# Performance work log

Hardware: AMD Instinct MI355X
Metric: run time of the kernel (lower is better)

## Reference

```python
import jax, jax.numpy as jnp
import numpy as np

H = 2048          # hidden_size
HEAD = 64         # head_size
NH = H // HEAD    # n_heads = 32
B, T = 4, 4096
LORA_MIX = 32     # per-branch rank of time_maa low-rank mixer (5 branches)
LORA_DECAY = 64   # rank of decay low-rank mixer


def setup_inputs() -> dict:
    key = jax.random.key(0)
    ks = jax.random.split(key, 24)
    s = 0.02  # small init scale keeps tanh/silu in sane range
    inp = {
        "hidden": jax.random.normal(ks[0], (B, T, H), jnp.float32),
        "attn_x": jax.random.normal(ks[1], (B, H), jnp.float32),
        "attn_kv": jax.random.normal(ks[2], (B, NH, HEAD, HEAD), jnp.float32),
        "ffn_x": jax.random.normal(ks[3], (B, H), jnp.float32),
        "time_maa_x": jax.random.normal(ks[4], (1, 1, H), jnp.float32) * s,
        "time_maa_w": jax.random.normal(ks[5], (1, 1, H), jnp.float32) * s,
        "time_maa_k": jax.random.normal(ks[6], (1, 1, H), jnp.float32) * s,
        "time_maa_v": jax.random.normal(ks[7], (1, 1, H), jnp.float32) * s,
        "time_maa_r": jax.random.normal(ks[8], (1, 1, H), jnp.float32) * s,
        "time_maa_g": jax.random.normal(ks[9], (1, 1, H), jnp.float32) * s,
        "time_maa_w1": jax.random.normal(ks[10], (H, LORA_MIX * 5), jnp.float32) * s,
        "time_maa_w2": jax.random.normal(ks[11], (5, LORA_MIX, H), jnp.float32) * s,
        "time_decay": jax.random.normal(ks[12], (1, 1, H), jnp.float32) * s,
        "time_decay_w1": jax.random.normal(ks[13], (H, LORA_DECAY), jnp.float32) * s,
        "time_decay_w2": jax.random.normal(ks[14], (LORA_DECAY, H), jnp.float32) * s,
        "time_faaaa": jax.random.normal(ks[15], (NH, HEAD), jnp.float32) * s,
        "receptance_w": jax.random.normal(ks[16], (H, H), jnp.float32) * s,
        "key_w": jax.random.normal(ks[17], (H, H), jnp.float32) * s,
        "value_w": jax.random.normal(ks[18], (H, H), jnp.float32) * s,
        "gate_w": jax.random.normal(ks[19], (H, H), jnp.float32) * s,
        "output_w": jax.random.normal(ks[20], (H, H), jnp.float32) * s,
    }
    return inp


def reference(hidden, attn_x, attn_kv, ffn_x,
              time_maa_x, time_maa_w, time_maa_k, time_maa_v, time_maa_r, time_maa_g,
              time_maa_w1, time_maa_w2,
              time_decay, time_decay_w1, time_decay_w2, time_faaaa,
              receptance_w, key_w, value_w, gate_w, output_w):
    b, t, h = hidden.shape
    # token shift: prepend previous chunk's last token state
    shifted = jnp.concatenate([attn_x[:, None, :], hidden[:, :-1, :]], axis=1)  # [B,T,H]
    x = hidden
    xx = shifted - x
    # low-rank data-dependent mixing coefficients (5 branches)
    xxx = x + xx * time_maa_x                                        # [B,T,H]
    xxx = jnp.tanh(xxx.reshape(-1, h) @ time_maa_w1)                 # [B*T, 5*32]
    xxx = xxx.reshape(-1, 5, LORA_MIX).transpose(1, 0, 2)            # [5, B*T, 32]
    xxx = jnp.einsum('fnr,frh->fnh', xxx, time_maa_w2)               # [5, B*T, H]
    xxx = xxx.reshape(5, b, t, h)
    mw, mk, mv, mr, mg = xxx[0], xxx[1], xxx[2], xxx[3], xxx[4]
    # note: source uses additive mix (x + xx + coeff), faithful to code as written
    td_in = x + xx + (time_maa_w + mw)
    k_in = x + xx + (time_maa_k + mk)
    v_in = x + xx + (time_maa_v + mv)
    r_in = x + xx + (time_maa_r + mr)
    g_in = x + xx + (time_maa_g + mg)
    receptance = jnp.einsum('bth,hd->btd', r_in, receptance_w)
    key = jnp.einsum('bth,hd->btd', k_in, key_w)
    value = jnp.einsum('bth,hd->btd', v_in, value_w)
    gate = jax.nn.silu(jnp.einsum('bth,hd->btd', g_in, gate_w))
    td = jnp.tanh(jnp.einsum('bth,hr->btr', td_in, time_decay_w1))
    td = jnp.einsum('btr,rh->bth', td, time_decay_w2)
    td = time_decay + td                                              # [B,T,H] per-channel decay
    attn_x_new = hidden[:, -1]                                        # [B,H]
    return (receptance, key, value, gate, td, attn_x_new)
```

## Files before the change

kernel.cpp:

```cpp
#include <hip/hip_runtime.h>

#define H 2048
#define TT 4096
#define BB 4
#define NROWS (BB * TT)
#define NTH ((size_t)NROWS * H)
#define KCAT (H + 32)
#define KC8  (H + 64)
#define NTH64 ((size_t)NROWS * 64)

typedef __attribute__((ext_vector_type(8))) short bh8;
typedef __attribute__((ext_vector_type(4))) float f32x4;

__device__ inline unsigned short f2bf(float f) {
    union { float f; unsigned u; } v; v.f = f;
    unsigned r = v.u + 0x7fff + ((v.u >> 16) & 1);
    return (unsigned short)(r >> 16);
}
__device__ inline float bf2f(unsigned short u) {
    union { unsigned u; float f; } v; v.u = ((unsigned)u) << 16; return v.f;
}
__device__ inline void gload_lds16(const void* g, void* l) {
    __builtin_amdgcn_global_load_lds(
        (const __attribute__((address_space(1))) void*)g,
        (__attribute__((address_space(3))) void*)l, 16, 0, 0);
}

__global__ __launch_bounds__(256) void prep_kernel(
    const float* __restrict__ hidden, const float* __restrict__ attn_x,
    const float* __restrict__ tmx,
    unsigned short* __restrict__ shifted, unsigned short* __restrict__ xin,
    float* __restrict__ out5) {
    size_t i = ((size_t)blockIdx.x * 256 + threadIdx.x) * 4;
    int n = (int)(i >> 11);
    int h = (int)(i & 2047);
    int t = n & (TT - 1);
    float4 x = *(const float4*)(hidden + i);
    float4 s;
    if (t == 0) {
        int b = n >> 12;
        s = *(const float4*)(attn_x + ((size_t)b << 11) + h);
    } else {
        s = *(const float4*)(hidden + (i - H));
    }
    float4 m = *(const float4*)(tmx + h);
    ushort4 sh, xi;
    sh.x = f2bf(s.x); sh.y = f2bf(s.y); sh.z = f2bf(s.z); sh.w = f2bf(s.w);
    xi.x = f2bf(x.x + (s.x - x.x) * m.x);
    xi.y = f2bf(x.y + (s.y - x.y) * m.y);
    xi.z = f2bf(x.z + (s.z - x.z) * m.z);
    xi.w = f2bf(x.w + (s.w - x.w) * m.w);
    *(ushort4*)(shifted + i) = sh;
    *(ushort4*)(xin + i) = xi;
    if (t == TT - 1) {
        int b = n >> 12;
        *(float4*)(out5 + ((size_t)b << 11) + h) = x;
    }
}

__global__ __launch_bounds__(256) void transpose_kernel(
    const float* __restrict__ in, unsigned short* __restrict__ outp,
    int R, int C, int ldo) {
    __shared__ float tile[32][33];
    int tx = threadIdx.x & 31, ty = threadIdx.x >> 5;
    int r0 = blockIdx.y * 32, c0 = blockIdx.x * 32;
    for (int i = ty; i < 32; i += 8) {
        int r = r0 + i, c = c0 + tx;
        tile[i][tx] = (r < R && c < C) ? in[(size_t)r * C + c] : 0.f;
    }
    __syncthreads();
    for (int i = ty; i < 32; i += 8) {
        int c = c0 + i, r = r0 + tx;
        if (c < C && r < R) outp[(size_t)c * ldo + r] = f2bf(tile[tx][i]);
    }
}

__global__ __launch_bounds__(256) void transpose4_kernel(
    const float* __restrict__ w0, const float* __restrict__ w1,
    const float* __restrict__ w2, const float* __restrict__ w3,
    unsigned short* __restrict__ d0, unsigned short* __restrict__ d1,
    unsigned short* __restrict__ d2, unsigned short* __restrict__ d3) {
    __shared__ float tile[32][33];
    int bz = blockIdx.z;
    const float* in = bz == 0 ? w0 : bz == 1 ? w1 : bz == 2 ? w2 : w3;
    unsigned short* outp = bz == 0 ? d0 : bz == 1 ? d1 : bz == 2 ? d2 : d3;
    int tx = threadIdx.x & 31, ty = threadIdx.x >> 5;
    int r0 = blockIdx.y * 32, c0 = blockIdx.x * 32;
    for (int i = ty; i < 32; i += 8)
        tile[i][tx] = in[(size_t)(r0 + i) * H + c0 + tx];
    __syncthreads();
    for (int i = ty; i < 32; i += 8)
        outp[(size_t)(c0 + i) * KC8 + r0 + tx] = f2bf(tile[tx][i]);
}

__global__ __launch_bounds__(256) void w2wp_kernel(
    const float* __restrict__ W2,
    const float* __restrict__ w0, const float* __restrict__ w1,
    const float* __restrict__ w2, const float* __restrict__ w3,
    const float* __restrict__ W1d,
    const float* __restrict__ mR, const float* __restrict__ mK,
    const float* __restrict__ mV, const float* __restrict__ mG,
    const float* __restrict__ mW,
    float* __restrict__ part) {
    const int br = blockIdx.z, ks = blockIdx.y, dblk = blockIdx.x;
    const int tid = threadIdx.x;
    const float* W; int D; const float* maa;
    if (br < 4) {
        W = br == 0 ? w0 : br == 1 ? w1 : br == 2 ? w2 : w3; D = H;
        maa = br == 0 ? mR : br == 1 ? mK : br == 2 ? mV : mG;
    } else { W = W1d; D = 64; maa = mW; }
    const int f = br < 4 ? ((0x4213 >> (br * 4)) & 15) : 0;
    const float* W2f = W2 + (size_t)f * 32 * H;
    __shared__ float w2s[256][33];
    const int k0 = ks * 256;
#pragma unroll
    for (int r = 0; r < 33; ++r)
        w2s[tid][r] = (r < 32) ? W2f[(size_t)r * H + k0 + tid] : maa[k0 + tid];
    __syncthreads();
    int d = dblk * 256 + tid;
    if (d >= D) return;
    float a[33];
#pragma unroll
    for (int r = 0; r < 33; ++r) a[r] = 0.f;
    for (int kk = 0; kk < 256; ++kk) {
        float w = W[(size_t)(k0 + kk) * D + d];
        const float* ws2 = w2s[kk];
#pragma unroll
        for (int r = 0; r < 33; ++r) a[r] += ws2[r] * w;
    }
    float* pp = part + (((size_t)br * 8 + ks) * 33) * 2048 + d;
#pragma unroll
    for (int r = 0; r < 33; ++r) pp[(size_t)r * 2048] = a[r];
}

__global__ __launch_bounds__(256) void w2wr_kernel(
    const float* __restrict__ part,
    unsigned short* __restrict__ dR, unsigned short* __restrict__ dK,
    unsigned short* __restrict__ dV, unsigned short* __restrict__ dG,
    unsigned short* __restrict__ d1,
    float* __restrict__ bias4, float* __restrict__ bias0) {
    int gid = blockIdx.x * 256 + threadIdx.x;
    if (gid < 262144) {
        int br = gid >> 16, rem = gid & 65535;
        int r = rem >> 11, d = rem & 2047;
        float s = 0.f;
#pragma unroll
        for (int ks = 0; ks < 8; ++ks)
            s += part[(((size_t)br * 8 + ks) * 33 + r) * 2048 + d];
        unsigned short* dst = br == 0 ? dR : br == 1 ? dK : br == 2 ? dV : dG;
        dst[(size_t)d * KC8 + H + r] = f2bf(s);
        dst[(size_t)d * KC8 + H + 32 + r] = 0;
    } else if (gid < 264192) {
        int q = gid - 262144;
        int r = q >> 6, d = q & 63;
        float s = 0.f;
#pragma unroll
        for (int ks = 0; ks < 8; ++ks)
            s += part[(((size_t)4 * 8 + ks) * 33 + r) * 2048 + d];
        d1[(size_t)d * KCAT + H + r] = f2bf(s);
    } else if (gid < 272384) {
        int q = gid - 264192;
        int br = q >> 11, d = q & 2047;
        float s = 0.f;
#pragma unroll
        for (int ks = 0; ks < 8; ++ks)
            s += part[(((size_t)br * 8 + ks) * 33 + 32) * 2048 + d];
        bias4[br * H + d] = s;
    } else if (gid < 272448) {
        int d = gid - 272384;
        float s = 0.f;
#pragma unroll
        for (int ks = 0; ks < 8; ++ks)
            s += part[(((size_t)4 * 8 + ks) * 33 + 32) * 2048 + d];
        bias0[d] = s;
    }
}

template <int WM, int WN, int FM, int FN, int HAS_BIAS, int ACT, int OF32, int ZPAD>
__global__ __launch_bounds__(256) void gemm_kernel(
    const unsigned short* __restrict__ A, int lda,
    const unsigned short* __restrict__ A2, int lda2, int KS,
    const unsigned short* __restrict__ Bt, int ldb, int K,
    void* __restrict__ outp, int ldo, int NT,
    const float* __restrict__ bias) {
    static_assert(WM * WN == 4, "4 waves");
    constexpr int BM = WM * FM * 16;
    constexpr int BN = WN * FN * 16;
    __shared__ unsigned short As[BM * 32];
    __shared__ unsigned short Bs[BN * 32];

    const int nb = gridDim.x;
    const int bid = blockIdx.x;
    const int swz = (bid & 7) * (nb >> 3) + (bid >> 3);
    const int mt = swz / NT, nt = swz % NT;
    const int m0 = mt * BM, n0 = nt * BN;

    const int tid = threadIdx.x;
    const int wave = tid >> 6, lane = tid & 63;
    const int l16 = lane & 15, kh = lane >> 4;
    const int wr = wave / WN, wc = wave % WN;

    f32x4 acc[FM][FN] = {};

    constexpr int ACH = BM * 4;
    constexpr int BCH = BN * 4;

    for (int k0 = 0; k0 < K; k0 += 32) {
#pragma unroll
        for (int i = 0; i < (ACH + 255) / 256; ++i) {
            int c = i * 256 + tid;
            if (ACH % 256 == 0 || c < ACH) {
                int row = c >> 2, ck = c & 3;
                int kk = k0 + ck * 8;
                const unsigned short* gp = (kk < KS)
                    ? A  + (size_t)(m0 + row) * lda  + kk
                    : A2 + (size_t)(m0 + row) * lda2 + (kk - KS);
                gload_lds16(gp, As + (size_t)(i * 256 + wave * 64) * 8);
            }
        }
#pragma unroll
        for (int i = 0; i < (BCH + 255) / 256; ++i) {
            int c = i * 256 + tid;
            if (BCH % 256 == 0 || c < BCH) {
                int row = c >> 2, ck = c & 3;
                gload_lds16(Bt + (size_t)(n0 + row) * ldb + k0 + ck * 8,
                            Bs + (size_t)(i * 256 + wave * 64) * 8);
            }
        }
        __syncthreads();
        bh8 av[FM], bv[FN];
#pragma unroll
        for (int mi = 0; mi < FM; ++mi)
            av[mi] = *(const bh8*)((const char*)As + (((wr * FM + mi) * 16 + l16) * 64 + kh * 16));
#pragma unroll
        for (int ni = 0; ni < FN; ++ni)
            bv[ni] = *(const bh8*)((const char*)Bs + (((wc * FN + ni) * 16 + l16) * 64 + kh * 16));
#pragma unroll
        for (int mi = 0; mi < FM; ++mi)
#pragma unroll
            for (int ni = 0; ni < FN; ++ni)
                acc[mi][ni] = __builtin_amdgcn_mfma_f32_16x16x32_bf16(
                    av[mi], bv[ni], acc[mi][ni], 0, 0, 0);
        __syncthreads();
    }

#pragma unroll
    for (int mi = 0; mi < FM; ++mi) {
#pragma unroll
        for (int ni = 0; ni < FN; ++ni) {
            int col = n0 + (wc * FN + ni) * 16 + l16;
            float bcol = HAS_BIAS ? bias[col] : 0.f;
#pragma unroll
            for (int j = 0; j < 4; ++j) {
                int row = m0 + (wr * FM + mi) * 16 + kh * 4 + j;
                float v = acc[mi][ni][j] + bcol;
                if (ACT == 1) v = v * (1.f / (1.f + __expf(-v)));
                else if (ACT == 2) v = tanhf(v);
                if (ZPAD) {
                    int br = col >> 5, cc = col & 31;
                    unsigned short* zp = (unsigned short*)outp
                        + (size_t)br * NTH64 + (size_t)row * 64 + cc;
                    zp[0] = f2bf(v);
                    zp[32] = 0;
                } else if (OF32) {
                    ((float*)outp)[(size_t)row * ldo + col] = v;
                } else {
                    ((unsigned short*)outp)[(size_t)row * ldo + col] = f2bf(v);
                }
            }
        }
    }
}

__global__ __launch_bounds__(512, 2) void bigproj8_kernel(
    const unsigned short* __restrict__ A,
    const unsigned short* __restrict__ zpad,
    const unsigned short* __restrict__ bt0, const unsigned short* __restrict__ bt1,
    const unsigned short* __restrict__ bt2, const unsigned short* __restrict__ bt3,
    const unsigned short* __restrict__ Bcat1,
    const float* __restrict__ bias4, const float* __restrict__ bias0,
    float* __restrict__ out, float* __restrict__ tdmid) {
    constexpr int BUFB = 32768;
    constexpr int NTK = KC8 / 32;
    __shared__ alignas(16) char lds[4 * BUFB];

    const int tid = threadIdx.x;
    const int wave = tid >> 6, lane = tid & 63;
    const int l16 = lane & 15, kh = lane >> 4;
    const int kh16 = kh * 16;

    if (blockIdx.x < 128) {
        unsigned short* As = (unsigned short*)lds;
        unsigned short* Bs = (unsigned short*)(lds + 8192);
        const int m0 = blockIdx.x * 128;
        f32x4 acc[4] = {};
        const int rowS = tid >> 2, ckS = tid & 3;
        for (int k0 = 0; k0 < KCAT; k0 += 32) {
            {
                int kk = k0 + ckS * 8;
                const unsigned short* gp = (kk < H)
                    ? A    + (size_t)(m0 + rowS) * H + kk
                    : zpad + (size_t)(m0 + rowS) * 64 + (kk - H);
                gload_lds16(gp, As + (size_t)(wave * 64) * 8);
            }
            if (tid < 256) {
                gload_lds16(Bcat1 + (size_t)rowS * KCAT + k0 + ckS * 8,
                            Bs + (size_t)(wave * 64) * 8);
            }
            __syncthreads();
            bh8 av = *(const bh8*)((const char*)As + ((wave * 16 + l16) * 64 + kh16));
#pragma unroll
            for (int ni = 0; ni < 4; ++ni) {
                bh8 bv = *(const bh8*)((const char*)Bs + ((ni * 16 + l16) * 64 + kh16));
                acc[ni] = __builtin_amdgcn_mfma_f32_16x16x32_bf16(av, bv, acc[ni], 0, 0, 0);
            }
            __syncthreads();
        }
#pragma unroll
        for (int ni = 0; ni < 4; ++ni) {
            int col = ni * 16 + l16;
            float bc = bias0[col];
#pragma unroll
            for (int j = 0; j < 4; ++j) {
                int row = m0 + wave * 16 + kh * 4 + j;
                tdmid[(size_t)row * 64 + col] = tanhf(acc[ni][j] + bc);
            }
        }
        return;
    }

    const int bid = blockIdx.x - 128;
    const int swz = (bid & 7) * 256 + (bid >> 3);
    const int branch = swz >> 9;
    const int tile = swz & 511;
    const int m0 = (tile >> 3) * 256, n0 = (tile & 7) * 256;

    const unsigned short* Bt = branch == 0 ? bt0 : branch == 1 ? bt1
                             : branch == 2 ? bt2 : bt3;
    const int f = (0x4213 >> (branch * 4)) & 15;
    const unsigned short* Az = zpad + (size_t)f * NTH64;

    const int wm = wave >> 2, wn = wave & 3;
    const int swr = (l16 & 8) << 2;

    const int rS = tid >> 2;
    const int kbx = ((tid & 3) * 16) ^ ((rS & 8) << 2);
    const char* bA0 = (const char*)A  + (size_t)(m0 + rS) * 4096 + kbx;
    const char* bA1 = bA0 + (size_t)128 * 4096;
    const char* bz0 = (const char*)Az + (size_t)(m0 + rS) * 128 + kbx;
    const char* bz1 = bz0 + (size_t)128 * 128;
    const char* bB0 = (const char*)Bt + (size_t)(n0 + rS) * (KC8 * 2) + kbx;
    const char* bB1 = bB0 + (size_t)128 * (KC8 * 2);
    const int dA0 = wave * 1024, dA1 = 8192 + wave * 1024;

    auto stageA = [&](int kt, char* nb) {
        const char *p0, *p1;
        if (kt < 64) { size_t o = (size_t)kt * 64;        p0 = bA0 + o; p1 = bA1 + o; }
        else         { size_t o = (size_t)(kt - 64) * 64; p0 = bz0 + o; p1 = bz1 + o; }
        gload_lds16(p0, nb + dA0);
        gload_lds16(p1, nb + dA1);
    };
    auto stageB = [&](int kt, char* nb) {
        size_t o = (size_t)kt * 64;
        gload_lds16(bB0 + o, nb + 16384 + dA0);
        gload_lds16(bB1 + o, nb + 16384 + dA1);
    };

    f32x4 acc[8][4] = {};
    bh8 avlo[4], avhi[4], bvA[4], bvB[4];

    stageA(0, lds);        stageB(0, lds);
    stageA(1, lds + BUFB); stageB(1, lds + BUFB);
    asm volatile("s_waitcnt vmcnt(4)" ::: "memory");
    __builtin_amdgcn_s_barrier();
    __builtin_amdgcn_sched_barrier(0);
#pragma unroll
    for (int i = 0; i < 4; ++i) {
        avlo[i] = *(const bh8*)(lds + (wm * 8 + i) * 1024 + l16 * 64 + (kh16 ^ swr));
        bvA[i]  = *(const bh8*)(lds + 16384 + (wn * 4 + i) * 1024 + l16 * 64 + (kh16 ^ swr));
    }

    auto tile_step = [&](int t, bh8 (&bvC)[4], bh8 (&bvN)[4]) {
        const char* Ab = lds + (t & 3) * BUFB;
        char* nb = lds + ((t + 2) & 3) * BUFB;
        const bool doSt = (t + 2) < NTK;

#pragma unroll
        for (int i = 0; i < 4; ++i)
            avhi[i] = *(const bh8*)(Ab + (wm * 8 + 4 + i) * 1024 + l16 * 64 + (kh16 ^ swr));
        if (doSt) stageA(t + 2, nb);
        __builtin_amdgcn_s_setprio(1);
#pragma unroll
        for (int mi = 0; mi < 4; ++mi)
#pragma unroll
            for (int ni = 0; ni < 4; ++ni)
                acc[mi][ni] = __builtin_amdgcn_mfma_f32_16x16x32_bf16(
                    avlo[mi], bvC[ni], acc[mi][ni], 0, 0, 0);
        __builtin_amdgcn_s_setprio(0);

        if (doSt) stageB(t + 2, nb);
        if (t + 1 < NTK) {
            if (doSt) asm volatile("s_waitcnt vmcnt(4)" ::: "memory");
            else      asm volatile("s_waitcnt vmcnt(0)" ::: "memory");
            __builtin_amdgcn_s_barrier();
            __builtin_amdgcn_sched_barrier(0);
            const char* Ab1 = lds + ((t + 1) & 3) * BUFB;
#pragma unroll
            for (int i = 0; i < 4; ++i) {
                avlo[i] = *(const bh8*)(Ab1 + (wm * 8 + i) * 1024 + l16 * 64 + (kh16 ^ swr));
                bvN[i]  = *(const bh8*)(Ab1 + 16384 + (wn * 4 + i) * 1024 + l16 * 64 + (kh16 ^ swr));
            }
        }
        __builtin_amdgcn_s_setprio(1);
#pragma unroll
        for (int mi = 0; mi < 4; ++mi)
#pragma unroll
            for (int ni = 0; ni < 4; ++ni)
                acc[4 + mi][ni] = __builtin_amdgcn_mfma_f32_16x16x32_bf16(
                    avhi[mi], bvC[ni], acc[4 + mi][ni], 0, 0, 0);
        __builtin_amdgcn_s_setprio(0);
    };

    for (int t = 0; t < NTK; t += 2) {
        tile_step(t,     bvA, bvB);
        tile_step(t + 1, bvB, bvA);
    }

    float* outp = out + (size_t)branch * NTH;
    const float* bias = bias4 + branch * H;
#pragma unroll
    for (int a = 0; a < 8; ++a) {
#pragma unroll
        for (int b = 0; b < 4; ++b) {
            int col = n0 + wn * 64 + b * 16 + l16;
            float bc = bias[col];
#pragma unroll
            for (int j = 0; j < 4; ++j) {
                int row = m0 + wm * 128 + a * 16 + kh * 4 + j;
                float v = acc[a][b][j] + bc;
                if (branch == 3) v = v * (1.f / (1.f + __expf(-v)));
                outp[(size_t)row * H + col] = v;
            }
        }
    }
}

__global__ __launch_bounds__(256) void td2_kernel(
    const float* __restrict__ tdmid, const float* __restrict__ W2d,
    const float* __restrict__ tdecay, float* __restrict__ outp) {
    int col = blockIdx.x * 256 + threadIdx.x;
    int row0 = blockIdx.y * 8;
    float a[8] = {0, 0, 0, 0, 0, 0, 0, 0};
    for (int r = 0; r < 64; ++r) {
        float w = W2d[(size_t)r * H + col];
#pragma unroll
        for (int j = 0; j < 8; ++j)
            a[j] += tdmid[(size_t)(row0 + j) * 64 + r] * w;
    }
    float b = tdecay[col];
#pragma unroll
    for (int j = 0; j < 8; ++j)
        outp[(size_t)(row0 + j) * H + col] = a[j] + b;
}

extern "C" void kernel_launch(void* const* d_in, const int* in_sizes, int n_in,
                              void* d_out, int out_size, void* d_ws, size_t ws_size,
                              hipStream_t stream) {
    const float* hidden = (const float*)d_in[0];
    const float* attn_x = (const float*)d_in[1];
    const float* tmx    = (const float*)d_in[4];
    const float* tmaa_w = (const float*)d_in[5];
    const float* tmaa_k = (const float*)d_in[6];
    const float* tmaa_v = (const float*)d_in[7];
    const float* tmaa_r = (const float*)d_in[8];
    const float* tmaa_g = (const float*)d_in[9];
    const float* W1     = (const float*)d_in[10];
    const float* W2     = (const float*)d_in[11];
    const float* tdecay = (const float*)d_in[12];
    const float* W1d    = (const float*)d_in[13];
    const float* W2d    = (const float*)d_in[14];
    const float* Wr     = (const float*)d_in[16];
    const float* Wk     = (const float*)d_in[17];
    const float* Wv     = (const float*)d_in[18];
    const float* Wg     = (const float*)d_in[19];

    float* out = (float*)d_out;

    char* ws = (char*)d_ws;
    size_t off = 0;
    auto alloc = [&](size_t bytes) {
        char* p = ws + off;
        off = (off + bytes + 255) & ~(size_t)255;
        return p;
    };
    unsigned short* shifted = (unsigned short*)alloc(NTH * 2);
    unsigned short* xin     = (unsigned short*)alloc(NTH * 2);
    unsigned short* zpad    = (unsigned short*)alloc(5 * NTH64 * 2);
    unsigned short* W1t     = (unsigned short*)alloc((size_t)160 * H * 2);
    unsigned short* BcatR   = (unsigned short*)alloc((size_t)H * KC8 * 2);
    unsigned short* BcatK   = (unsigned short*)alloc((size_t)H * KC8 * 2);
    unsigned short* BcatV   = (unsigned short*)alloc((size_t)H * KC8 * 2);
    unsigned short* BcatG   = (unsigned short*)alloc((size_t)H * KC8 * 2);
    unsigned short* Bcat1   = (unsigned short*)alloc((size_t)64 * KCAT * 2);
    float* tdmid            = (float*)alloc((size_t)NROWS * 64 * 4);
    float* part             = (float*)alloc((size_t)5 * 8 * 33 * 2048 * 4);
    float* bias4            = (float*)alloc(4 * H * 4);
    float* bias0            = (float*)alloc(64 * 4);

    prep_kernel<<<(unsigned)(NTH / (4 * 256)), 256, 0, stream>>>(
        hidden, attn_x, tmx, shifted, xin, out + 5 * NTH);

    transpose4_kernel<<<dim3(64, 64, 4), 256, 0, stream>>>(
        Wr, Wk, Wv, Wg, BcatR, BcatK, BcatV, BcatG);
    transpose_kernel<<<dim3(5, 64), 256, 0, stream>>>(W1, W1t, H, 160, H);
    transpose_kernel<<<dim3(2, 64), 256, 0, stream>>>(W1d, Bcat1, H, 64, KCAT);
    w2wp_kernel<<<dim3(8, 8, 5), 256, 0, stream>>>(
        W2, Wr, Wk, Wv, Wg, W1d,
        tmaa_r, tmaa_k, tmaa_v, tmaa_g, tmaa_w, part);
    w2wr_kernel<<<1065, 256, 0, stream>>>(
        part, BcatR, BcatK, BcatV, BcatG, Bcat1, bias4, bias0);

    gemm_kernel<4, 1, 1, 10, 0, 2, 0, 1><<<256, 256, 0, stream>>>(
        xin, H, xin, H, H, W1t, H, H, zpad, 0, 1, nullptr);

    bigproj8_kernel<<<2176, 512, 0, stream>>>(
        shifted, zpad, BcatR, BcatK, BcatV, BcatG, Bcat1,
        bias4, bias0, out, tdmid);

    td2_kernel<<<dim3(8, NROWS / 8), 256, 0, stream>>>(
        tdmid, W2d, tdecay, out + 4 * NTH);
}
```

Baseline: 853.6 us.

## Fuse decay second-stage projection into bigproj and merge weight transposes

The tanh decay intermediate now stays in LDS inside the first 128 blocks of bigproj8. Those blocks compute the 64-to-2048 decay projection and write the decay output directly, which removes the separate td2 kernel and its tdmid global round trip. The hope is that this scalar work overlaps with the large GEMM blocks. The cost is much less parallelism for that stage: 128 blocks now do what 16384 blocks did before, which risks a long tail. Separately, the three weight-transpose launches are merged into one launch indexed by blockIdx.z, with early exit for blocks beyond a matrix's column count.

Result: no change. 864.8 us (+1.3%).

```diff
diff --git a/kernel.cpp b/kernel.cpp
--- a/kernel.cpp
+++ b/kernel.cpp
@@ -58,39 +58,35 @@
     }
 }
 
-__global__ __launch_bounds__(256) void transpose_kernel(
-    const float* __restrict__ in, unsigned short* __restrict__ outp,
-    int R, int C, int ldo) {
+__global__ __launch_bounds__(256) void transpose_all_kernel(
+    const float* __restrict__ w0, const float* __restrict__ w1,
+    const float* __restrict__ w2, const float* __restrict__ w3,
+    const float* __restrict__ W1, const float* __restrict__ W1d,
+    unsigned short* __restrict__ d0, unsigned short* __restrict__ d1,
+    unsigned short* __restrict__ d2, unsigned short* __restrict__ d3,
+    unsigned short* __restrict__ W1t, unsigned short* __restrict__ dB1) {
     __shared__ float tile[32][33];
+    int bz = blockIdx.z;
+    const float* in; unsigned short* outp; int C, ldo;
+    if (bz < 4) {
+        in = bz == 0 ? w0 : bz == 1 ? w1 : bz == 2 ? w2 : w3;
+        outp = bz == 0 ? d0 : bz == 1 ? d1 : bz == 2 ? d2 : d3;
+        C = H; ldo = KC8;
+    } else if (bz == 4) { in = W1;  outp = W1t; C = 160; ldo = H; }
+    else                { in = W1d; outp = dB1; C = 64;  ldo = KCAT; }
+    int c0 = blockIdx.x * 32;
+    if (c0 >= C) return;
     int tx = threadIdx.x & 31, ty = threadIdx.x >> 5;
-    int r0 = blockIdx.y * 32, c0 = blockIdx.x * 32;
+    int r0 = blockIdx.y * 32;
     for (int i = ty; i < 32; i += 8) {
-        int r = r0 + i, c = c0 + tx;
-        tile[i][tx] = (r < R && c < C) ? in[(size_t)r * C + c] : 0.f;
+        int c = c0 + tx;
+        tile[i][tx] = (c < C) ? in[(size_t)(r0 + i) * C + c] : 0.f;
     }
     __syncthreads();
     for (int i = ty; i < 32; i += 8) {
-        int c = c0 + i, r = r0 + tx;
-        if (c < C && r < R) outp[(size_t)c * ldo + r] = f2bf(tile[tx][i]);
-    }
-}
-
-__global__ __launch_bounds__(256) void transpose4_kernel(
-    const float* __restrict__ w0, const float* __restrict__ w1,
-    const float* __restrict__ w2, const float* __restrict__ w3,
-    unsigned short* __restrict__ d0, unsigned short* __restrict__ d1,
-    unsigned short* __restrict__ d2, unsigned short* __restrict__ d3) {
-    __shared__ float tile[32][33];
-    int bz = blockIdx.z;
-    const float* in = bz == 0 ? w0 : bz == 1 ? w1 : bz == 2 ? w2 : w3;
-    unsigned short* outp = bz == 0 ? d0 : bz == 1 ? d1 : bz == 2 ? d2 : d3;
-    int tx = threadIdx.x & 31, ty = threadIdx.x >> 5;
-    int r0 = blockIdx.y * 32, c0 = blockIdx.x * 32;
-    for (int i = ty; i < 32; i += 8)
-        tile[i][tx] = in[(size_t)(r0 + i) * H + c0 + tx];
-    __syncthreads();
-    for (int i = ty; i < 32; i += 8)
-        outp[(size_t)(c0 + i) * KC8 + r0 + tx] = f2bf(tile[tx][i]);
+        int c = c0 + i;
+        if (c < C) outp[(size_t)c * ldo + r0 + tx] = f2bf(tile[tx][i]);
+    }
 }
 
 __global__ __launch_bounds__(256) void w2wp_kernel(
@@ -279,7 +275,8 @@
     const unsigned short* __restrict__ bt2, const unsigned short* __restrict__ bt3,
     const unsigned short* __restrict__ Bcat1,
     const float* __restrict__ bias4, const float* __restrict__ bias0,
-    float* __restrict__ out, float* __restrict__ tdmid) {
+    const float* __restrict__ W2d, const float* __restrict__ tdecay,
+    float* __restrict__ out) {
     constexpr int BUFB = 32768;
     constexpr int NTK = KC8 / 32;
     __shared__ alignas(16) char lds[4 * BUFB];
@@ -292,6 +289,7 @@
     if (blockIdx.x < 128) {
         unsigned short* As = (unsigned short*)lds;
         unsigned short* Bs = (unsigned short*)(lds + 8192);
+        float* tdlds = (float*)(lds + 16384);
         const int m0 = blockIdx.x * 128;
         f32x4 acc[4] = {};
         const int rowS = tid >> 2, ckS = tid & 3;
@@ -322,8 +320,26 @@
             float bc = bias0[col];
 #pragma unroll
             for (int j = 0; j < 4; ++j) {
-                int row = m0 + wave * 16 + kh * 4 + j;
-                tdmid[(size_t)row * 64 + col] = tanhf(acc[ni][j] + bc);
+                int row = wave * 16 + kh * 4 + j;
+                tdlds[row * 64 + col] = tanhf(acc[ni][j] + bc);
+            }
+        }
+        __syncthreads();
+        float* out4 = out + 4 * NTH + (size_t)m0 * H;
+        for (int cc = 0; cc < 4; ++cc) {
+            int col = cc * 512 + tid;
+            float b = tdecay[col];
+            for (int rg = 0; rg < 16; ++rg) {
+                float a[8] = {0, 0, 0, 0, 0, 0, 0, 0};
+                for (int r = 0; r < 64; ++r) {
+                    float w = W2d[(size_t)r * H + col];
+#pragma unroll
+                    for (int j = 0; j < 8; ++j)
+                        a[j] += tdlds[(rg * 8 + j) * 64 + r] * w;
+                }
+#pragma unroll
+                for (int j = 0; j < 8; ++j)
+                    out4[(size_t)(rg * 8 + j) * H + col] = a[j] + b;
             }
         }
         return;
@@ -443,24 +459,6 @@
             }
         }
     }
-}
-
-__global__ __launch_bounds__(256) void td2_kernel(
-    const float* __restrict__ tdmid, const float* __restrict__ W2d,
-    const float* __restrict__ tdecay, float* __restrict__ outp) {
-    int col = blockIdx.x * 256 + threadIdx.x;
-    int row0 = blockIdx.y * 8;
-    float a[8] = {0, 0, 0, 0, 0, 0, 0, 0};
-    for (int r = 0; r < 64; ++r) {
-        float w = W2d[(size_t)r * H + col];
-#pragma unroll
-        for (int j = 0; j < 8; ++j)
-            a[j] += tdmid[(size_t)(row0 + j) * 64 + r] * w;
-    }
-    float b = tdecay[col];
-#pragma unroll
-    for (int j = 0; j < 8; ++j)
-        outp[(size_t)(row0 + j) * H + col] = a[j] + b;
 }
 
 extern "C" void kernel_launch(void* const* d_in, const int* in_sizes, int n_in,
@@ -502,7 +500,6 @@
     unsigned short* BcatV   = (unsigned short*)alloc((size_t)H * KC8 * 2);
     unsigned short* BcatG   = (unsigned short*)alloc((size_t)H * KC8 * 2);
     unsigned short* Bcat1   = (unsigned short*)alloc((size_t)64 * KCAT * 2);
-    float* tdmid            = (float*)alloc((size_t)NROWS * 64 * 4);
     float* part             = (float*)alloc((size_t)5 * 8 * 33 * 2048 * 4);
     float* bias4            = (float*)alloc(4 * H * 4);
     float* bias0            = (float*)alloc(64 * 4);
@@ -510,10 +507,9 @@
     prep_kernel<<<(unsigned)(NTH / (4 * 256)), 256, 0, stream>>>(
         hidden, attn_x, tmx, shifted, xin, out + 5 * NTH);
 
-    transpose4_kernel<<<dim3(64, 64, 4), 256, 0, stream>>>(
-        Wr, Wk, Wv, Wg, BcatR, BcatK, BcatV, BcatG);
-    transpose_kernel<<<dim3(5, 64), 256, 0, stream>>>(W1, W1t, H, 160, H);
-    transpose_kernel<<<dim3(2, 64), 256, 0, stream>>>(W1d, Bcat1, H, 64, KCAT);
+    transpose_all_kernel<<<dim3(64, 64, 6), 256, 0, stream>>>(
+        Wr, Wk, Wv, Wg, W1, W1d,
+        BcatR, BcatK, BcatV, BcatG, W1t, Bcat1);
     w2wp_kernel<<<dim3(8, 8, 5), 256, 0, stream>>>(
         W2, Wr, Wk, Wv, Wg, W1d,
         tmaa_r, tmaa_k, tmaa_v, tmaa_g, tmaa_w, part);
@@ -525,8 +521,5 @@
 
     bigproj8_kernel<<<2176, 512, 0, stream>>>(
         shifted, zpad, BcatR, BcatK, BcatV, BcatG, Bcat1,
-        bias4, bias0, out, tdmid);
-
-    td2_kernel<<<dim3(8, NROWS / 8), 256, 0, stream>>>(
-        tdmid, W2d, tdecay, out + 4 * NTH);
-}
+        bias4, bias0, W2d, tdecay, out);
+}
```
